# Performance work log

Hardware: AMD Instinct MI355X
Metric: run time of the kernel (lower is better)

## Reference

```python
import jax, jax.numpy as jnp
import numpy as np

N_STEPS = 8  # DGL GatedGraphConv n_steps as hardcoded in GatedGCN.__init__


def _gru(a, h, Wih, Whh, bih, bhh):
    # torch.nn.GRUCell: gate order (r, z, n)
    gi = a @ Wih.T + bih          # [N, 3d]
    gh = h @ Whh.T + bhh          # [N, 3d]
    ir, iz, inn = jnp.split(gi, 3, axis=-1)
    hr, hz, hn = jnp.split(gh, 3, axis=-1)
    r = jax.nn.sigmoid(ir + hr)
    z = jax.nn.sigmoid(iz + hz)
    n = jnp.tanh(inn + r * hn)
    return (1.0 - z) * n + z * h


def _gated_conv(h, src, dst, W, b, Wih, Whh, bih, bhh):
    # DGL GatedGraphConv with a single etype: for each step,
    # message = Linear(h[src]); aggregate = sum over in-edges; h = GRU(agg, h)
    N = h.shape[0]

    def step(h, _):
        m = h @ W.T + b                                   # [N, d] linear per node (message fn)
        agg = jax.ops.segment_sum(m[src], dst, num_segments=N)  # [N, d] sum over in-edges
        return _gru(agg, h, Wih, Whh, bih, bhh), None

    h, _ = jax.lax.scan(step, h, None, length=N_STEPS)
    return h


def setup_inputs() -> dict:
    key = jax.random.key(0)
    ks = jax.random.split(key, 10)
    N, E, D = 50000, 800000, 128  # in_feats = h_feats = num_classes = 128
    s = 1.0 / np.sqrt(D)
    return {
        "in_feat": jax.random.normal(ks[0], (N, D), jnp.float32),
        "src": jax.random.randint(ks[1], (E,), 0, N),
        "dst": jax.random.randint(ks[2], (E,), 0, N),
        "W1": jax.random.normal(ks[3], (D, D), jnp.float32) * s,
        "b1": jnp.zeros((D,), jnp.float32),
        "Wih1": jax.random.normal(ks[4], (3 * D, D), jnp.float32) * s,
        "Whh1": jax.random.normal(ks[5], (3 * D, D), jnp.float32) * s,
        "bih1": jnp.zeros((3 * D,), jnp.float32),
        "bhh1": jnp.zeros((3 * D,), jnp.float32),
        "W2": jax.random.normal(ks[6], (D, D), jnp.float32) * s,
        "b2": jnp.zeros((D,), jnp.float32),
        "Wih2": jax.random.normal(ks[7], (3 * D, D), jnp.float32) * s,
        "Whh2": jax.random.normal(ks[8], (3 * D, D), jnp.float32) * s,
        "bih2": jnp.zeros((3 * D,), jnp.float32),
        "bhh2": jnp.zeros((3 * D,), jnp.float32),
    }


def reference(in_feat, src, dst, W1, b1, Wih1, Whh1, bih1, bhh1,
              W2, b2, Wih2, Whh2, bih2, bhh2):
    # in_feats == h_feats so DGL's zero-padding of the input is a no-op here.
    h = _gated_conv(in_feat, src, dst, W1, b1, Wih1, Whh1, bih1, bhh1)
    h = jax.nn.relu(h)
    h = _gated_conv(h, src, dst, W2, b2, Wih2, Whh2, bih2, bhh2)
    # dgl.mean_nodes with a single graph -> [1, num_classes]
    return jnp.mean(h, axis=0, keepdims=True)
```

## Files before the change

### kernel.cpp

```cpp
#include <hip/hip_runtime.h>
#include <hip/hip_bf16.h>
#include <cmath>

#define DD 128

typedef __attribute__((ext_vector_type(8))) short short8v;
typedef __attribute__((ext_vector_type(4))) float floatx4;

__device__ __forceinline__ float sigmoid_f(float x) { return 1.0f / (1.0f + __expf(-x)); }
__device__ __forceinline__ float tanh_f(float x) {
  float e = __expf(2.0f * x);
  return 1.0f - 2.0f / (e + 1.0f);
}
__device__ __forceinline__ unsigned short f2bf(float x) {
  __hip_bfloat16 b = __float2bfloat16(x);
  return *reinterpret_cast<unsigned short*>(&b);
}
__device__ __forceinline__ float bf2f(unsigned short s) {
  return __uint_as_float(((unsigned int)s) << 16);
}

__global__ __launch_bounds__(256) void deg_count(const int* __restrict__ dst,
                                                 int* __restrict__ deg, int E) {
  int e = blockIdx.x * blockDim.x + threadIdx.x;
  if (e < E) atomicAdd(&deg[dst[e]], 1);
}

__global__ __launch_bounds__(256) void scan_part(const int* __restrict__ deg,
                                                 int* __restrict__ bsum, int N) {
  __shared__ int s[256];
  int tid = threadIdx.x;
  int i = blockIdx.x * 256 + tid;
  s[tid] = (i < N) ? deg[i] : 0;
  __syncthreads();
  for (int st = 128; st > 0; st >>= 1) {
    if (tid < st) s[tid] += s[tid + st];
    __syncthreads();
  }
  if (tid == 0) bsum[blockIdx.x] = s[0];
}

__global__ __launch_bounds__(256) void scan_top(const int* __restrict__ bsum,
                                                int* __restrict__ bofs, int nb) {
  __shared__ int s[256];
  int tid = threadIdx.x;
  int v = (tid < nb) ? bsum[tid] : 0;
  s[tid] = v;
  __syncthreads();
  for (int o = 1; o < 256; o <<= 1) {
    int t = (tid >= o) ? s[tid - o] : 0;
    __syncthreads();
    s[tid] += t;
    __syncthreads();
  }
  if (tid < nb) bofs[tid] = s[tid] - v;
  if (tid == nb - 1) bofs[nb] = s[tid];
}

__global__ __launch_bounds__(256) void scan_final(const int* __restrict__ deg,
                                                  const int* __restrict__ bofs,
                                                  int* __restrict__ ofs,
                                                  int* __restrict__ cur, int N) {
  __shared__ int s[256];
  int tid = threadIdx.x;
  int i = blockIdx.x * 256 + tid;
  int v = (i < N) ? deg[i] : 0;
  s[tid] = v;
  __syncthreads();
  for (int o = 1; o < 256; o <<= 1) {
    int t = (tid >= o) ? s[tid - o] : 0;
    __syncthreads();
    s[tid] += t;
    __syncthreads();
  }
  int off = bofs[blockIdx.x] + s[tid] - v;
  if (i < N) {
    ofs[i] = off;
    cur[i] = off;
    if (i == N - 1) ofs[N] = off + v;
  }
}

__global__ __launch_bounds__(256) void fill_csr(const int* __restrict__ src,
                                                const int* __restrict__ dst,
                                                int* __restrict__ cur,
                                                int* __restrict__ eidx, int E) {
  int e = blockIdx.x * blockDim.x + threadIdx.x;
  if (e < E) {
    int p = atomicAdd(&cur[dst[e]], 1);
    eidx[p] = src[e];
  }
}

__global__ __launch_bounds__(128) void fuse_w(const float* __restrict__ Wih,
                                              const float* __restrict__ W,
                                              float* __restrict__ Wc32) {
  int r = blockIdx.x;
  int k = threadIdx.x;
  float acc = 0.0f;
  for (int j = 0; j < DD; ++j) acc = fmaf(Wih[r * DD + j], W[j * DD + k], acc);
  Wc32[(size_t)r * DD + k] = acc;
}

__global__ __launch_bounds__(128) void fuse_u(const float* __restrict__ Wih,
                                              const float* __restrict__ b,
                                              float* __restrict__ u) {
  int r = blockIdx.x * 128 + threadIdx.x;
  if (r < 3 * DD) {
    float acc = 0.0f;
    for (int j = 0; j < DD; ++j) acc = fmaf(Wih[r * DD + j], b[j], acc);
    u[r] = acc;
  }
}

__global__ __launch_bounds__(256) void split_w(const float* __restrict__ Wf,
                                               const float* __restrict__ Whh,
                                               unsigned short* __restrict__ Wp) {
  int i = blockIdx.x * 256 + threadIdx.x;
  const int TOT = 6 * DD * DD;
  if (i < TOT) {
    int r = i >> 7;
    float x = (r < 3 * DD) ? Wf[i] : Whh[i - 3 * DD * DD];
    unsigned short hb = f2bf(x);
    float xr = x - bf2f(hb);
    unsigned short mb = f2bf(xr);
    Wp[i] = hb;
    Wp[TOT + i] = mb;
  }
}

__global__ __launch_bounds__(256) void gather_h(const float* __restrict__ h,
                                                const int* __restrict__ ofs,
                                                const int* __restrict__ eidx,
                                                float* __restrict__ agg, int N) {
  int node = blockIdx.x * 8 + (threadIdx.x >> 5);
  if (node >= N) return;
  int l = (threadIdx.x & 31) << 2;
  int beg = ofs[node], end = ofs[node + 1];
  float4 aa[4];
#pragma unroll
  for (int j = 0; j < 4; ++j) aa[j] = (float4){0.f, 0.f, 0.f, 0.f};
  int e = beg;
  for (; e + 7 < end; e += 8) {
    float4 v[8];
#pragma unroll
    for (int j = 0; j < 8; ++j)
      v[j] = *(const float4*)(h + (size_t)eidx[e + j] * DD + l);
#pragma unroll
    for (int j = 0; j < 8; ++j) {
      aa[j & 3].x += v[j].x; aa[j & 3].y += v[j].y;
      aa[j & 3].z += v[j].z; aa[j & 3].w += v[j].w;
    }
  }
  for (; e + 1 < end; e += 2) {
    float4 v0 = *(const float4*)(h + (size_t)eidx[e] * DD + l);
    float4 v1 = *(const float4*)(h + (size_t)eidx[e + 1] * DD + l);
    aa[0].x += v0.x; aa[0].y += v0.y; aa[0].z += v0.z; aa[0].w += v0.w;
    aa[1].x += v1.x; aa[1].y += v1.y; aa[1].z += v1.z; aa[1].w += v1.w;
  }
  if (e < end) {
    float4 v = *(const float4*)(h + (size_t)eidx[e] * DD + l);
    aa[0].x += v.x; aa[0].y += v.y; aa[0].z += v.z; aa[0].w += v.w;
  }
  float4 r;
  r.x = (aa[0].x + aa[1].x) + (aa[2].x + aa[3].x);
  r.y = (aa[0].y + aa[1].y) + (aa[2].y + aa[3].y);
  r.z = (aa[0].z + aa[1].z) + (aa[2].z + aa[3].z);
  r.w = (aa[0].w + aa[1].w) + (aa[2].w + aa[3].w);
  *(float4*)(agg + (size_t)node * DD + l) = r;
}

__device__ __forceinline__ void split8_2(const float* p, short8v& q0, short8v& q1) {
  float4 v0 = *(const float4*)(p);
  float4 v1 = *(const float4*)(p + 4);
  float f[8] = {v0.x, v0.y, v0.z, v0.w, v1.x, v1.y, v1.z, v1.w};
#pragma unroll
  for (int e = 0; e < 8; ++e) {
    float x = f[e];
    unsigned short hb = f2bf(x);
    float xr = x - bf2f(hb);
    q0[e] = (short)hb;
    q1[e] = (short)f2bf(xr);
  }
}

__global__ __launch_bounds__(256, 2) void gru_mfma3(
    const float* __restrict__ Agg, const float* __restrict__ H,
    const unsigned short* __restrict__ Wp,
    const float* __restrict__ bih, const float* __restrict__ bhh,
    const float* __restrict__ u, const int* __restrict__ deg,
    float* __restrict__ Hout, int N, int do_relu)
{
  __shared__ short sB[2][96 * DD];
  const int TOT = 6 * DD * DD;
  const int tid = threadIdx.x;
  const int wid = tid >> 6;
  const int lane = tid & 63;
  const int lrow = lane & 15;
  const int hi = lane >> 4;
  const int lk = hi * 8;
  const int rowBase = blockIdx.x * 128 + wid * 32;
  const int j0 = blockIdx.y * 32;

  floatx4 acc[6][2][2];
#pragma unroll
  for (int g = 0; g < 6; ++g)
#pragma unroll
    for (int ct = 0; ct < 2; ++ct)
#pragma unroll
      for (int rt = 0; rt < 2; ++rt) acc[g][ct][rt] = (floatx4){0.f, 0.f, 0.f, 0.f};

  int r0 = rowBase + lrow;       if (r0 >= N) r0 = N - 1;
  int r1 = rowBase + 16 + lrow;  if (r1 >= N) r1 = N - 1;

  int s_row[6], s_cnk[6];
  size_t s_grow[6];
#pragma unroll
  for (int i = 0; i < 6; ++i) {
    int ch = tid + i * 256;
    s_row[i] = ch >> 4;
    s_cnk[i] = ch & 15;
    s_grow[i] = (size_t)((s_row[i] >> 5) * DD + j0 + (s_row[i] & 31));
  }

  short8v wreg[12];
#pragma unroll
  for (int i = 0; i < 6; ++i) {
    wreg[i]     = *(const short8v*)(Wp + 0 * TOT + s_grow[i] * DD + s_cnk[i] * 8);
    wreg[6 + i] = *(const short8v*)(Wp + 1 * TOT + s_grow[i] * DD + s_cnk[i] * 8);
  }

  short8v frag[2][4][2];
#pragma unroll
  for (int kc = 0; kc < 4; ++kc) {
    split8_2(Agg + (size_t)r0 * DD + kc * 32 + lk, frag[0][kc][0], frag[1][kc][0]);
    split8_2(Agg + (size_t)r1 * DD + kc * 32 + lk, frag[0][kc][1], frag[1][kc][1]);
  }

#pragma unroll
  for (int arr = 0; arr < 2; ++arr) {
    if (arr > 0) __syncthreads();
#pragma unroll
    for (int i = 0; i < 6; ++i) {
      int off = s_row[i] * DD + (s_cnk[i] ^ (s_row[i] & 7)) * 8;
      *(short8v*)(&sB[0][off]) = wreg[i];
      *(short8v*)(&sB[1][off]) = wreg[6 + i];
    }
    if (arr == 0) {
      const size_t g1 = (size_t)384 * DD;
#pragma unroll
      for (int i = 0; i < 6; ++i) {
        wreg[i]     = *(const short8v*)(Wp + 0 * TOT + g1 + s_grow[i] * DD + s_cnk[i] * 8);
        wreg[6 + i] = *(const short8v*)(Wp + 1 * TOT + g1 + s_grow[i] * DD + s_cnk[i] * 8);
      }
    }
    __syncthreads();

    __builtin_amdgcn_s_setprio(1);
#pragma unroll
    for (int kc = 0; kc < 4; ++kc) {
#pragma unroll
      for (int gl = 0; gl < 3; ++gl) {
#pragma unroll
        for (int ct = 0; ct < 2; ++ct) {
          int lr = gl * 32 + ct * 16 + lrow;
          int off = lr * DD + ((kc * 4 + hi) ^ (lr & 7)) * 8;
          short8v bh = *(const short8v*)(&sB[0][off]);
#pragma unroll
          for (int rt = 0; rt < 2; ++rt) {
            acc[arr * 3 + gl][ct][rt] = __builtin_amdgcn_mfma_f32_16x16x32_bf16(
                frag[0][kc][rt], bh, acc[arr * 3 + gl][ct][rt], 0, 0, 0);
            acc[arr * 3 + gl][ct][rt] = __builtin_amdgcn_mfma_f32_16x16x32_bf16(
                frag[1][kc][rt], bh, acc[arr * 3 + gl][ct][rt], 0, 0, 0);
          }
          short8v bm = *(const short8v*)(&sB[1][off]);
#pragma unroll
          for (int rt = 0; rt < 2; ++rt) {
            acc[arr * 3 + gl][ct][rt] = __builtin_amdgcn_mfma_f32_16x16x32_bf16(
                frag[0][kc][rt], bm, acc[arr * 3 + gl][ct][rt], 0, 0, 0);
          }
        }
      }
    }
    __builtin_amdgcn_s_setprio(0);

    if (arr == 0) {
#pragma unroll
      for (int kc = 0; kc < 4; ++kc) {
        split8_2(H + (size_t)r0 * DD + kc * 32 + lk, frag[0][kc][0], frag[1][kc][0]);
        split8_2(H + (size_t)r1 * DD + kc * 32 + lk, frag[0][kc][1], frag[1][kc][1]);
      }
    }
  }

  float bi_r[2], bi_z[2], bi_n[2], bh_r[2], bh_z[2], bh_n[2], u_r[2], u_z[2], u_n[2];
#pragma unroll
  for (int ct = 0; ct < 2; ++ct) {
    int c = j0 + ct * 16 + lrow;
    bi_r[ct] = bih[c];  bi_z[ct] = bih[DD + c];  bi_n[ct] = bih[2 * DD + c];
    bh_r[ct] = bhh[c];  bh_z[ct] = bhh[DD + c];  bh_n[ct] = bhh[2 * DD + c];
    u_r[ct]  = u[c];    u_z[ct]  = u[DD + c];    u_n[ct]  = u[2 * DD + c];
  }

#pragma unroll
  for (int rt = 0; rt < 2; ++rt) {
#pragma unroll
    for (int q = 0; q < 4; ++q) {
      int row = rowBase + rt * 16 + hi * 4 + q;
      if (row < N) {
        float dg = (float)deg[row];
#pragma unroll
        for (int ct = 0; ct < 2; ++ct) {
          int c = j0 + ct * 16 + lrow;
          float ir = acc[0][ct][rt][q] + bi_r[ct] + dg * u_r[ct];
          float iz = acc[1][ct][rt][q] + bi_z[ct] + dg * u_z[ct];
          float in = acc[2][ct][rt][q] + bi_n[ct] + dg * u_n[ct];
          float hr = acc[3][ct][rt][q] + bh_r[ct];
          float hz = acc[4][ct][rt][q] + bh_z[ct];
          float hn = acc[5][ct][rt][q] + bh_n[ct];
          float rg = sigmoid_f(ir + hr);
          float zg = sigmoid_f(iz + hz);
          float ng = tanh_f(in + rg * hn);
          float hold = H[(size_t)row * DD + c];
          float out = (1.0f - zg) * ng + zg * hold;
          if (do_relu) out = fmaxf(out, 0.0f);
          Hout[(size_t)row * DD + c] = out;
        }
      }
    }
  }
}

__global__ __launch_bounds__(256) void col_mean(
    const float* __restrict__ H, float* __restrict__ out, int N)
{
  __shared__ float s[256];
  int c = threadIdx.x & 127;
  int rg = threadIdx.x >> 7;
  float acc = 0.0f;
  for (int r = blockIdx.x * 2 + rg; r < N; r += gridDim.x * 2)
    acc += H[(size_t)r * DD + c];
  s[threadIdx.x] = acc;
  __syncthreads();
  if (threadIdx.x < 128) {
    float v = (s[threadIdx.x] + s[threadIdx.x + 128]) * (1.0f / (float)N);
    unsafeAtomicAdd(out + c, v);
  }
}

extern "C" void kernel_launch(void* const* d_in, const int* in_sizes, int n_in,
                              void* d_out, int out_size, void* d_ws, size_t ws_size,
                              hipStream_t stream) {
  const float* in_feat = (const float*)d_in[0];
  const int* src = (const int*)d_in[1];
  const int* dst = (const int*)d_in[2];
  const float* W[2]   = {(const float*)d_in[3], (const float*)d_in[9]};
  const float* bb[2]  = {(const float*)d_in[4], (const float*)d_in[10]};
  const float* Wih[2] = {(const float*)d_in[5], (const float*)d_in[11]};
  const float* Whh[2] = {(const float*)d_in[6], (const float*)d_in[12]};
  const float* bih[2] = {(const float*)d_in[7], (const float*)d_in[13]};
  const float* bhh[2] = {(const float*)d_in[8], (const float*)d_in[14]};
  const int N = in_sizes[0] / DD;
  const int E = in_sizes[1];

  const size_t nd = (size_t)N * DD;
  char* base = (char*)d_ws;
  float* hA  = (float*)base; base += nd * sizeof(float);
  float* hB  = (float*)base; base += nd * sizeof(float);
  float* agg = (float*)base; base += nd * sizeof(float);
  float* Wc32 = (float*)base; base += (size_t)3 * DD * DD * sizeof(float);
  unsigned short* Wp[2];
  Wp[0] = (unsigned short*)base; base += (size_t)2 * 6 * DD * DD * sizeof(unsigned short);
  Wp[1] = (unsigned short*)base; base += (size_t)2 * 6 * DD * DD * sizeof(unsigned short);
  float* u[2];
  u[0] = (float*)base; base += 3 * DD * sizeof(float);
  u[1] = (float*)base; base += 3 * DD * sizeof(float);
  int* deg  = (int*)base; base += (size_t)N * sizeof(int);
  int* ofs  = (int*)base; base += ((size_t)N + 1) * sizeof(int);
  int* cur  = (int*)base; base += (size_t)N * sizeof(int);
  int* eidx = (int*)base; base += (size_t)E * sizeof(int);
  int* bsum = (int*)base; base += 256 * sizeof(int);
  int* bofs = (int*)base; base += 257 * sizeof(int);

  const int nb = (N + 255) / 256;

  hipMemsetAsync(deg, 0, (size_t)N * sizeof(int), stream);
  deg_count<<<(E + 255) / 256, 256, 0, stream>>>(dst, deg, E);
  scan_part<<<nb, 256, 0, stream>>>(deg, bsum, N);
  scan_top<<<1, 256, 0, stream>>>(bsum, bofs, nb);
  scan_final<<<nb, 256, 0, stream>>>(deg, bofs, ofs, cur, N);
  fill_csr<<<(E + 255) / 256, 256, 0, stream>>>(src, dst, cur, eidx, E);

  for (int layer = 0; layer < 2; ++layer) {
    fuse_w<<<3 * DD, 128, 0, stream>>>(Wih[layer], W[layer], Wc32);
    split_w<<<(6 * DD * DD + 255) / 256, 256, 0, stream>>>(Wc32, Whh[layer], Wp[layer]);
    fuse_u<<<3, 128, 0, stream>>>(Wih[layer], bb[layer], u[layer]);
  }

  hipMemcpyAsync(hA, in_feat, nd * sizeof(float), hipMemcpyDeviceToDevice, stream);

  float* hcur = hA;
  float* hnxt = hB;
  const int gblocks = (N + 7) / 8;
  const int mblocks = (N + 127) / 128;

  for (int layer = 0; layer < 2; ++layer) {
    for (int step_i = 0; step_i < 8; ++step_i) {
      gather_h<<<gblocks, 256, 0, stream>>>(hcur, ofs, eidx, agg, N);
      int do_relu = (layer == 0 && step_i == 7) ? 1 : 0;
      gru_mfma3<<<dim3(mblocks, 4), 256, 0, stream>>>(
          agg, hcur, Wp[layer], bih[layer], bhh[layer],
          u[layer], deg, hnxt, N, do_relu);
      float* t = hcur; hcur = hnxt; hnxt = t;
    }
  }

  hipMemsetAsync(d_out, 0, DD * sizeof(float), stream);
  col_mean<<<256, 256, 0, stream>>>(hcur, (float*)d_out, N);
}
```

Baseline: 1.966 ms.

## Stream A-fragments per k-chunk to cut registers and raise GRU kernel occupancy

The GRU MFMA kernel no longer holds the full split bf16 fragments for all four k-chunks or a register prefetch of the second weight half. Instead it loads and splits the activation rows one k-chunk at a time, prefetching the next chunk during the MFMAs. Weights are loaded directly before the LDS store for each half. Launch bounds rise from 2 to 3 blocks per CU. This trades the early weight and H prefetch overlap for lower register pressure and higher occupancy.

```diff
diff --git a/kernel.cpp b/kernel.cpp
--- a/kernel.cpp
+++ b/kernel.cpp
@@ -170,9 +170,7 @@
   *(float4*)(agg + (size_t)node * DD + l) = r;
 }
 
-__device__ __forceinline__ void split8_2(const float* p, short8v& q0, short8v& q1) {
-  float4 v0 = *(const float4*)(p);
-  float4 v1 = *(const float4*)(p + 4);
+__device__ __forceinline__ void split8_2v(float4 v0, float4 v1, short8v& q0, short8v& q1) {
   float f[8] = {v0.x, v0.y, v0.z, v0.w, v1.x, v1.y, v1.z, v1.w};
 #pragma unroll
   for (int e = 0; e < 8; ++e) {
@@ -184,7 +182,7 @@
   }
 }
 
-__global__ __launch_bounds__(256, 2) void gru_mfma3(
+__global__ __launch_bounds__(256, 3) void gru_mfma3(
     const float* __restrict__ Agg, const float* __restrict__ H,
     const unsigned short* __restrict__ Wp,
     const float* __restrict__ bih, const float* __restrict__ bhh,
@@ -223,42 +221,48 @@
     s_grow[i] = (size_t)((s_row[i] >> 5) * DD + j0 + (s_row[i] & 31));
   }
 
-  short8v wreg[12];
-#pragma unroll
-  for (int i = 0; i < 6; ++i) {
-    wreg[i]     = *(const short8v*)(Wp + 0 * TOT + s_grow[i] * DD + s_cnk[i] * 8);
-    wreg[6 + i] = *(const short8v*)(Wp + 1 * TOT + s_grow[i] * DD + s_cnk[i] * 8);
-  }
-
-  short8v frag[2][4][2];
-#pragma unroll
-  for (int kc = 0; kc < 4; ++kc) {
-    split8_2(Agg + (size_t)r0 * DD + kc * 32 + lk, frag[0][kc][0], frag[1][kc][0]);
-    split8_2(Agg + (size_t)r1 * DD + kc * 32 + lk, frag[0][kc][1], frag[1][kc][1]);
-  }
-
 #pragma unroll
   for (int arr = 0; arr < 2; ++arr) {
+    const size_t gbase = (size_t)arr * 384 * DD;
     if (arr > 0) __syncthreads();
-#pragma unroll
-    for (int i = 0; i < 6; ++i) {
-      int off = s_row[i] * DD + (s_cnk[i] ^ (s_row[i] & 7)) * 8;
-      *(short8v*)(&sB[0][off]) = wreg[i];
-      *(short8v*)(&sB[1][off]) = wreg[6 + i];
-    }
-    if (arr == 0) {
-      const size_t g1 = (size_t)384 * DD;
+
+    {
+      short8v w0[6], w1[6];
 #pragma unroll
       for (int i = 0; i < 6; ++i) {
-        wreg[i]     = *(const short8v*)(Wp + 0 * TOT + g1 + s_grow[i] * DD + s_cnk[i] * 8);
-        wreg[6 + i] = *(const short8v*)(Wp + 1 * TOT + g1 + s_grow[i] * DD + s_cnk[i] * 8);
+        w0[i] = *(const short8v*)(Wp + 0 * TOT + gbase + s_grow[i] * DD + s_cnk[i] * 8);
+        w1[i] = *(const short8v*)(Wp + 1 * TOT + gbase + s_grow[i] * DD + s_cnk[i] * 8);
+      }
+#pragma unroll
+      for (int i = 0; i < 6; ++i) {
+        int off = s_row[i] * DD + (s_cnk[i] ^ (s_row[i] & 7)) * 8;
+        *(short8v*)(&sB[0][off]) = w0[i];
+        *(short8v*)(&sB[1][off]) = w1[i];
       }
     }
     __syncthreads();
 
+    const float* A0 = (arr ? H : Agg) + (size_t)r0 * DD + lk;
+    const float* A1 = (arr ? H : Agg) + (size_t)r1 * DD + lk;
+
+    float4 pa0 = *(const float4*)(A0);
+    float4 pa1 = *(const float4*)(A0 + 4);
+    float4 pb0 = *(const float4*)(A1);
+    float4 pb1 = *(const float4*)(A1 + 4);
+
     __builtin_amdgcn_s_setprio(1);
 #pragma unroll
     for (int kc = 0; kc < 4; ++kc) {
+      float4 qa0, qa1, qb0, qb1;
+      if (kc < 3) {
+        qa0 = *(const float4*)(A0 + (kc + 1) * 32);
+        qa1 = *(const float4*)(A0 + (kc + 1) * 32 + 4);
+        qb0 = *(const float4*)(A1 + (kc + 1) * 32);
+        qb1 = *(const float4*)(A1 + (kc + 1) * 32 + 4);
+      }
+      short8v f00, f10, f01, f11;
+      split8_2v(pa0, pa1, f00, f10);
+      split8_2v(pb0, pb1, f01, f11);
 #pragma unroll
       for (int gl = 0; gl < 3; ++gl) {
 #pragma unroll
@@ -266,31 +270,24 @@
           int lr = gl * 32 + ct * 16 + lrow;
           int off = lr * DD + ((kc * 4 + hi) ^ (lr & 7)) * 8;
           short8v bh = *(const short8v*)(&sB[0][off]);
-#pragma unroll
-          for (int rt = 0; rt < 2; ++rt) {
-            acc[arr * 3 + gl][ct][rt] = __builtin_amdgcn_mfma_f32_16x16x32_bf16(
-                frag[0][kc][rt], bh, acc[arr * 3 + gl][ct][rt], 0, 0, 0);
-            acc[arr * 3 + gl][ct][rt] = __builtin_amdgcn_mfma_f32_16x16x32_bf16(
-                frag[1][kc][rt], bh, acc[arr * 3 + gl][ct][rt], 0, 0, 0);
-          }
+          acc[arr * 3 + gl][ct][0] = __builtin_amdgcn_mfma_f32_16x16x32_bf16(
+              f00, bh, acc[arr * 3 + gl][ct][0], 0, 0, 0);
+          acc[arr * 3 + gl][ct][0] = __builtin_amdgcn_mfma_f32_16x16x32_bf16(
+              f10, bh, acc[arr * 3 + gl][ct][0], 0, 0, 0);
+          acc[arr * 3 + gl][ct][1] = __builtin_amdgcn_mfma_f32_16x16x32_bf16(
+              f01, bh, acc[arr * 3 + gl][ct][1], 0, 0, 0);
+          acc[arr * 3 + gl][ct][1] = __builtin_amdgcn_mfma_f32_16x16x32_bf16(
+              f11, bh, acc[arr * 3 + gl][ct][1], 0, 0, 0);
           short8v bm = *(const short8v*)(&sB[1][off]);
-#pragma unroll
-          for (int rt = 0; rt < 2; ++rt) {
-            acc[arr * 3 + gl][ct][rt] = __builtin_amdgcn_mfma_f32_16x16x32_bf16(
-                frag[0][kc][rt], bm, acc[arr * 3 + gl][ct][rt], 0, 0, 0);
-          }
+          acc[arr * 3 + gl][ct][0] = __builtin_amdgcn_mfma_f32_16x16x32_bf16(
+              f00, bm, acc[arr * 3 + gl][ct][0], 0, 0, 0);
+          acc[arr * 3 + gl][ct][1] = __builtin_amdgcn_mfma_f32_16x16x32_bf16(
+              f01, bm, acc[arr * 3 + gl][ct][1], 0, 0, 0);
         }
       }
+      if (kc < 3) { pa0 = qa0; pa1 = qa1; pb0 = qb0; pb1 = qb1; }
     }
     __builtin_amdgcn_s_setprio(0);
-
-    if (arr == 0) {
-#pragma unroll
-      for (int kc = 0; kc < 4; ++kc) {
-        split8_2(H + (size_t)r0 * DD + kc * 32 + lk, frag[0][kc][0], frag[1][kc][0]);
-        split8_2(H + (size_t)r1 * DD + kc * 32 + lk, frag[0][kc][1], frag[1][kc][1]);
-      }
-    }
   }
 
   float bi_r[2], bi_z[2], bi_n[2], bh_r[2], bh_z[2], bh_n[2], u_r[2], u_z[2], u_n[2];
```

Result: faster. 1.840 ms (-6.4%).
